# Optimization experiments

Measured on AMD Instinct MI355X. Metric: run time of the kernel, lower is better.

The kernel has to match this reference:

```python
import jax, jax.numpy as jnp
import numpy as np

B, T, H, DFF = 32, 4096, 512, 512  # hidden_size=512, d_ff=512, h feature dim = 2*H


def setup_inputs() -> dict:
    key = jax.random.key(0)
    ks = jax.random.split(key, 8)
    sc = 0.02
    return {
        "s": jax.random.normal(ks[0], (B, H), dtype=jnp.float32),
        "h": jax.random.normal(ks[1], (B, T, 2 * H), dtype=jnp.float32),
        "W_a_w": jax.random.normal(ks[2], (DFF, H), dtype=jnp.float32) * sc,
        "W_a_b": jnp.zeros((DFF,), dtype=jnp.float32),
        "U_a_w": jax.random.normal(ks[3], (DFF, 2 * H), dtype=jnp.float32) * sc,
        "U_a_b": jnp.zeros((DFF,), dtype=jnp.float32),
        "V_a_w": jax.random.normal(ks[4], (1, DFF), dtype=jnp.float32) * sc,
        "V_a_b": jnp.zeros((1,), dtype=jnp.float32),
    }


def reference(s, h, W_a_w, W_a_b, U_a_w, U_a_b, V_a_w, V_a_b):
    # Bahdanau additive attention scoring (NOTE: original has no softmax).
    ws = s @ W_a_w.T + W_a_b                              # [B, d_ff]
    uh = jnp.einsum('bte,fe->btf', h, U_a_w) + U_a_b       # [B, T, d_ff]
    x = jnp.tanh(ws[:, None, :] + uh)                      # [B, T, d_ff]
    energy = x @ V_a_w[0] + V_a_b[0]                       # [B, T]
    context = jnp.einsum('bt,bte->be', energy, h)          # [B, 2*hidden]
    return context
```

## Files before the change

### kernel.cpp

```cpp
#include <hip/hip_runtime.h>
#include <cstdint>
#include <cstddef>

#define B_SZ 32
#define T_SZ 4096
#define H2   1024
#define DFF_ 512
#define TM   64
#define BK   32
#define NSTEP (H2 / BK)
#define PAD  8
#define LDB  (BK + PAD)

typedef __attribute__((ext_vector_type(8))) short bf16x8;
typedef __attribute__((ext_vector_type(4))) float f32x4;

__device__ __forceinline__ unsigned short f2bf(float x) {
  unsigned u = __float_as_uint(x);
  u += 0x7fffu + ((u >> 16) & 1u);
  return (unsigned short)(u >> 16);
}

__global__ void prep_u_kernel(const float* __restrict__ U,
                              unsigned short* __restrict__ Upk) {
  int g = blockIdx.x * 256 + threadIdx.x;
  int k  = g & 31;
  int f  = (g >> 5) & 511;
  int ks = g >> 14;
  float v = U[f * H2 + ks * 32 + k];
  Upk[(ks * DFF_ + f) * LDB + k] = f2bf(v);
}

__global__ void prep_ws_kernel(const float* __restrict__ s, const float* __restrict__ W,
                               const float* __restrict__ Wb, const float* __restrict__ Ub,
                               float* __restrict__ wsm) {
  int idx = blockIdx.x * 256 + threadIdx.x;
  int b = idx >> 9, f = idx & 511;
  const float4* s4 = (const float4*)(s + b * 512);
  const float4* w4 = (const float4*)(W + f * 512);
  float acc = 0.f;
  #pragma unroll 4
  for (int i = 0; i < 128; ++i) {
    float4 a = s4[i], w = w4[i];
    acc += a.x * w.x + a.y * w.y + a.z * w.z + a.w * w.w;
  }
  wsm[idx] = acc + Wb[f] + Ub[f];
}

__global__ __launch_bounds__(512) void attn_main(
    const float* __restrict__ h, const unsigned short* __restrict__ Upk,
    const float* __restrict__ wsm, const float* __restrict__ Vw,
    const float* __restrict__ Vb, float* __restrict__ out) {
  __shared__ unsigned short As[TM * LDB];
  __shared__ unsigned short Bs[DFF_ * LDB];
  __shared__ float ws_s[DFF_];
  __shared__ float V_s[DFF_];
  __shared__ float energy_s[TM];

  const int tid  = threadIdx.x;
  const int blk  = blockIdx.x;
  const int b    = blk >> 6;
  const int t0   = (blk & 63) * TM;
  const int lane = tid & 63;
  const int wave = tid >> 6;
  const int ln15 = lane & 15;
  const int q    = lane >> 4;
  const int r    = wave & 3;
  const int ch   = wave >> 2;

  ws_s[tid] = wsm[b * DFF_ + tid];
  V_s[tid]  = Vw[tid];
  if (tid < TM) energy_s[tid] = Vb[0];

  f32x4 acc[16];
  #pragma unroll
  for (int i = 0; i < 16; ++i) acc[i] = (f32x4){0.f, 0.f, 0.f, 0.f};

  const int arow = tid >> 3;
  const int ac4  = (tid & 7) * 4;
  const float* hbase = h + ((size_t)(b * T_SZ + t0)) * H2;

  for (int ks = 0; ks < NSTEP; ++ks) {
    __syncthreads();
    float4 av = *(const float4*)(hbase + (size_t)arow * H2 + ks * 32 + ac4);
    ushort4 ab;
    ab.x = f2bf(av.x); ab.y = f2bf(av.y); ab.z = f2bf(av.z); ab.w = f2bf(av.w);
    *(ushort4*)&As[arow * LDB + ac4] = ab;
    const char* gsrc = (const char*)(Upk + (size_t)ks * DFF_ * LDB);
    char* lbs = (char*)Bs;
    #pragma unroll
    for (int i = 0; i < 5; ++i) {
      int off = i * 8192 + tid * 16;
      __builtin_amdgcn_global_load_lds(
        (const __attribute__((address_space(1))) unsigned int*)(gsrc + off),
        (__attribute__((address_space(3))) unsigned int*)(lbs + off),
        16, 0, 0);
    }
    __syncthreads();
    bf16x8 af = *(const bf16x8*)&As[(r * 16 + ln15) * LDB + q * 8];
    #pragma unroll
    for (int ct = 0; ct < 16; ++ct) {
      bf16x8 bfr = *(const bf16x8*)&Bs[(ch * 256 + ct * 16 + ln15) * LDB + q * 8];
      acc[ct] = __builtin_amdgcn_mfma_f32_16x16x32_bf16(af, bfr, acc[ct], 0, 0, 0);
    }
  }

  float esum[4] = {0.f, 0.f, 0.f, 0.f};
  #pragma unroll
  for (int ct = 0; ct < 16; ++ct) {
    int f = ch * 256 + ct * 16 + ln15;
    float wsf = ws_s[f], vf = V_s[f];
    #pragma unroll
    for (int rg = 0; rg < 4; ++rg) {
      float z = wsf + acc[ct][rg];
      float e = __expf(2.f * z);
      float x = 1.f - 2.f / (e + 1.f);
      esum[rg] += x * vf;
    }
  }
  #pragma unroll
  for (int rg = 0; rg < 4; ++rg) {
    #pragma unroll
    for (int m = 1; m < 16; m <<= 1) esum[rg] += __shfl_xor(esum[rg], m, 64);
  }
  if (ln15 == 0) {
    #pragma unroll
    for (int rg = 0; rg < 4; ++rg)
      atomicAdd(&energy_s[r * 16 + q * 4 + rg], esum[rg]);
  }
  __syncthreads();

  int e0 = tid * 2;
  float c0 = 0.f, c1 = 0.f;
  const float2* h2p = (const float2*)hbase + (e0 >> 1);
  #pragma unroll 4
  for (int row = 0; row < TM; ++row) {
    float en = energy_s[row];
    float2 hv = h2p[(size_t)row * (H2 / 2)];
    c0 += en * hv.x;
    c1 += en * hv.y;
  }
  atomicAdd(&out[b * H2 + e0], c0);
  atomicAdd(&out[b * H2 + e0 + 1], c1);
}

extern "C" void kernel_launch(void* const* d_in, const int* in_sizes, int n_in,
                              void* d_out, int out_size, void* d_ws, size_t ws_size,
                              hipStream_t stream) {
  const float* s  = (const float*)d_in[0];
  const float* h  = (const float*)d_in[1];
  const float* Ww = (const float*)d_in[2];
  const float* Wb = (const float*)d_in[3];
  const float* Uw = (const float*)d_in[4];
  const float* Ub = (const float*)d_in[5];
  const float* Vw = (const float*)d_in[6];
  const float* Vb = (const float*)d_in[7];
  float* out = (float*)d_out;

  unsigned short* Upk = (unsigned short*)d_ws;
  float* wsm = (float*)((char*)d_ws + (size_t)NSTEP * DFF_ * LDB * 2);

  hipMemsetAsync(out, 0, (size_t)out_size * sizeof(float), stream);
  prep_u_kernel<<<(NSTEP * DFF_ * BK) / 256, 256, 0, stream>>>(Uw, Upk);
  prep_ws_kernel<<<(B_SZ * DFF_) / 256, 256, 0, stream>>>(s, Ww, Wb, Ub, wsm);
  attn_main<<<B_SZ * (T_SZ / TM), 512, 0, stream>>>(h, Upk, wsm, Vw, Vb, out);
}
```

Before: 903.0 us.

## Double-buffer LDS tiles, pre-swizzle U into MFMA fragment layout, retile waves

```diff
diff --git a/kernel.cpp b/kernel.cpp
--- a/kernel.cpp
+++ b/kernel.cpp
@@ -9,8 +9,6 @@
 #define TM   64
 #define BK   32
 #define NSTEP (H2 / BK)
-#define PAD  8
-#define LDB  (BK + PAD)
 
 typedef __attribute__((ext_vector_type(8))) short bf16x8;
 typedef __attribute__((ext_vector_type(4))) float f32x4;
@@ -24,11 +22,13 @@
 __global__ void prep_u_kernel(const float* __restrict__ U,
                               unsigned short* __restrict__ Upk) {
   int g = blockIdx.x * 256 + threadIdx.x;
-  int k  = g & 31;
-  int f  = (g >> 5) & 511;
+  int j  = g & 7;
+  int l  = (g >> 3) & 63;
+  int ct = (g >> 9) & 31;
   int ks = g >> 14;
-  float v = U[f * H2 + ks * 32 + k];
-  Upk[(ks * DFF_ + f) * LDB + k] = f2bf(v);
+  int f  = ct * 16 + (l & 15);
+  int k  = ks * 32 + (l >> 4) * 8 + j;
+  Upk[g] = f2bf(U[f * H2 + k]);
 }
 
 __global__ void prep_ws_kernel(const float* __restrict__ s, const float* __restrict__ W,
@@ -47,14 +47,15 @@
   wsm[idx] = acc + Wb[f] + Ub[f];
 }
 
-__global__ __launch_bounds__(512) void attn_main(
+__global__ __launch_bounds__(512, 4) void attn_main(
     const float* __restrict__ h, const unsigned short* __restrict__ Upk,
     const float* __restrict__ wsm, const float* __restrict__ Vw,
     const float* __restrict__ Vb, float* __restrict__ out) {
-  __shared__ unsigned short As[TM * LDB];
-  __shared__ unsigned short Bs[DFF_ * LDB];
+  __shared__ unsigned short Bs[2][NSTEP ? 32 * 64 * 8 : 1];
+  __shared__ unsigned short As[2][4 * 64 * 8];
   __shared__ float ws_s[DFF_];
   __shared__ float V_s[DFF_];
+  __shared__ float energy_part[8][TM];
   __shared__ float energy_s[TM];
 
   const int tid  = threadIdx.x;
@@ -62,71 +63,108 @@
   const int b    = blk >> 6;
   const int t0   = (blk & 63) * TM;
   const int lane = tid & 63;
-  const int wave = tid >> 6;
+  const int cg   = tid >> 6;
   const int ln15 = lane & 15;
-  const int q    = lane >> 4;
-  const int r    = wave & 3;
-  const int ch   = wave >> 2;
+  const int q4   = lane >> 4;
 
   ws_s[tid] = wsm[b * DFF_ + tid];
   V_s[tid]  = Vw[tid];
-  if (tid < TM) energy_s[tid] = Vb[0];
+
+  const int arow = tid >> 3;
+  const int ak   = (tid & 7) * 4;
+  const int a_off = (arow >> 4) * 512 + (ak >> 3) * 128 + (arow & 15) * 8 + (ak & 7);
+  const float* hbase = h + ((size_t)(b * T_SZ + t0)) * H2;
+  const float* aptr  = hbase + (size_t)arow * H2 + ak;
 
   f32x4 acc[16];
   #pragma unroll
   for (int i = 0; i < 16; ++i) acc[i] = (f32x4){0.f, 0.f, 0.f, 0.f};
 
-  const int arow = tid >> 3;
-  const int ac4  = (tid & 7) * 4;
-  const float* hbase = h + ((size_t)(b * T_SZ + t0)) * H2;
-
-  for (int ks = 0; ks < NSTEP; ++ks) {
-    __syncthreads();
-    float4 av = *(const float4*)(hbase + (size_t)arow * H2 + ks * 32 + ac4);
-    ushort4 ab;
-    ab.x = f2bf(av.x); ab.y = f2bf(av.y); ab.z = f2bf(av.z); ab.w = f2bf(av.w);
-    *(ushort4*)&As[arow * LDB + ac4] = ab;
-    const char* gsrc = (const char*)(Upk + (size_t)ks * DFF_ * LDB);
-    char* lbs = (char*)Bs;
-    #pragma unroll
-    for (int i = 0; i < 5; ++i) {
+  auto stageB = [&](int ks, int buf) {
+    const char* gsrc = (const char*)Upk + (size_t)ks * 32768;
+    char* ldst = (char*)&Bs[buf][0];
+    #pragma unroll
+    for (int i = 0; i < 4; ++i) {
       int off = i * 8192 + tid * 16;
       __builtin_amdgcn_global_load_lds(
         (const __attribute__((address_space(1))) unsigned int*)(gsrc + off),
-        (__attribute__((address_space(3))) unsigned int*)(lbs + off),
+        (__attribute__((address_space(3))) unsigned int*)(ldst + off),
         16, 0, 0);
     }
+  };
+  auto writeA = [&](float4 av, int buf) {
+    ushort4 ab;
+    ab.x = f2bf(av.x); ab.y = f2bf(av.y); ab.z = f2bf(av.z); ab.w = f2bf(av.w);
+    *(ushort4*)&As[buf][a_off] = ab;
+  };
+
+  stageB(0, 0);
+  {
+    float4 av0 = *(const float4*)(aptr);
+    writeA(av0, 0);
+  }
+  __syncthreads();
+
+  for (int ks = 0; ks < NSTEP; ++ks) {
+    const int cur = ks & 1;
+    float4 av;
+    if (ks < NSTEP - 1) {
+      stageB(ks + 1, cur ^ 1);
+      av = *(const float4*)(aptr + (ks + 1) * BK);
+    }
+    bf16x8 af[4];
+    #pragma unroll
+    for (int rt = 0; rt < 4; ++rt)
+      af[rt] = *(const bf16x8*)&As[cur][rt * 512 + lane * 8];
+    #pragma unroll
+    for (int ct2 = 0; ct2 < 4; ++ct2) {
+      int ct = cg * 4 + ct2;
+      bf16x8 bfr = *(const bf16x8*)&Bs[cur][(ct * 64 + lane) * 8];
+      #pragma unroll
+      for (int rt = 0; rt < 4; ++rt)
+        acc[ct2 * 4 + rt] =
+          __builtin_amdgcn_mfma_f32_16x16x32_bf16(af[rt], bfr, acc[ct2 * 4 + rt], 0, 0, 0);
+    }
+    if (ks < NSTEP - 1) writeA(av, cur ^ 1);
     __syncthreads();
-    bf16x8 af = *(const bf16x8*)&As[(r * 16 + ln15) * LDB + q * 8];
-    #pragma unroll
-    for (int ct = 0; ct < 16; ++ct) {
-      bf16x8 bfr = *(const bf16x8*)&Bs[(ch * 256 + ct * 16 + ln15) * LDB + q * 8];
-      acc[ct] = __builtin_amdgcn_mfma_f32_16x16x32_bf16(af, bfr, acc[ct], 0, 0, 0);
-    }
-  }
-
-  float esum[4] = {0.f, 0.f, 0.f, 0.f};
-  #pragma unroll
-  for (int ct = 0; ct < 16; ++ct) {
-    int f = ch * 256 + ct * 16 + ln15;
+  }
+
+  float esum[16];
+  #pragma unroll
+  for (int i = 0; i < 16; ++i) esum[i] = 0.f;
+  #pragma unroll
+  for (int ct2 = 0; ct2 < 4; ++ct2) {
+    int f = cg * 64 + ct2 * 16 + ln15;
     float wsf = ws_s[f], vf = V_s[f];
     #pragma unroll
-    for (int rg = 0; rg < 4; ++rg) {
-      float z = wsf + acc[ct][rg];
-      float e = __expf(2.f * z);
-      float x = 1.f - 2.f / (e + 1.f);
-      esum[rg] += x * vf;
-    }
-  }
-  #pragma unroll
-  for (int rg = 0; rg < 4; ++rg) {
-    #pragma unroll
-    for (int m = 1; m < 16; m <<= 1) esum[rg] += __shfl_xor(esum[rg], m, 64);
+    for (int rt = 0; rt < 4; ++rt) {
+      #pragma unroll
+      for (int rg = 0; rg < 4; ++rg) {
+        float z = wsf + acc[ct2 * 4 + rt][rg];
+        float e = __expf(2.f * z);
+        float x = 1.f - 2.f / (e + 1.f);
+        esum[rt * 4 + rg] += x * vf;
+      }
+    }
+  }
+  #pragma unroll
+  for (int i = 0; i < 16; ++i) {
+    #pragma unroll
+    for (int m = 1; m < 16; m <<= 1) esum[i] += __shfl_xor(esum[i], m, 64);
   }
   if (ln15 == 0) {
     #pragma unroll
-    for (int rg = 0; rg < 4; ++rg)
-      atomicAdd(&energy_s[r * 16 + q * 4 + rg], esum[rg]);
+    for (int rt = 0; rt < 4; ++rt)
+      #pragma unroll
+      for (int rg = 0; rg < 4; ++rg)
+        energy_part[cg][rt * 16 + q4 * 4 + rg] = esum[rt * 4 + rg];
+  }
+  __syncthreads();
+  if (tid < TM) {
+    float e = Vb[0];
+    #pragma unroll
+    for (int w = 0; w < 8; ++w) e += energy_part[w][tid];
+    energy_s[tid] = e;
   }
   __syncthreads();
 
@@ -158,10 +196,10 @@
   float* out = (float*)d_out;
 
   unsigned short* Upk = (unsigned short*)d_ws;
-  float* wsm = (float*)((char*)d_ws + (size_t)NSTEP * DFF_ * LDB * 2);
+  float* wsm = (float*)((char*)d_ws + (size_t)NSTEP * 32768);
 
   hipMemsetAsync(out, 0, (size_t)out_size * sizeof(float), stream);
-  prep_u_kernel<<<(NSTEP * DFF_ * BK) / 256, 256, 0, stream>>>(Uw, Upk);
+  prep_u_kernel<<<(DFF_ * H2) / 256, 256, 0, stream>>>(Uw, Upk);
   prep_ws_kernel<<<(B_SZ * DFF_) / 256, 256, 0, stream>>>(s, Ww, Wb, Ub, wsm);
   attn_main<<<B_SZ * (T_SZ / TM), 512, 0, stream>>>(h, Upk, wsm, Vw, Vb, out);
 }
```

New measurement: 899.3 us. About the same (-0.4%).
